# Optimization experiments

Hardware: AMD Instinct MI355X
Metric: run time of the kernel (lower is better)

The kernel has to match this reference:

```python
import jax, jax.numpy as jnp
import numpy as np

KS = 7          # kernel_size (odd)
STRIDE = 2
HALF = KS // 2  # window half-width
B, C, L = 32, 64, 4096


def setup_inputs() -> dict:
    key = jax.random.key(0)
    k1, k2 = jax.random.split(key)
    f = jax.random.normal(k1, (B, C, L), dtype=jnp.float32)
    # learned per-channel scale t ~ U(0, 4) (tiny epsilon to avoid div-by-zero)
    t = jax.random.uniform(k2, (C,), minval=0.0, maxval=4.0, dtype=jnp.float32) + 1e-3
    return {"f": f, "t": t}


def reference(f, t):
    b, c, n = f.shape
    # parabolic structuring function h[c, j] = -z_j^2 / (4 t_c), z = -HALF..HALF
    z = jnp.linspace(-HALF, HALF, KS, dtype=jnp.float32)
    h = -(z ** 2) / (4.0 * t[:, None])  # [C, KS]
    # morphological dilation (max-plus correlation) with -inf padding at borders
    pad = jnp.pad(f, ((0, 0), (0, 0), (HALF, HALF)), constant_values=-jnp.inf)
    out = pad[:, :, 0:n] + h[:, 0][None, :, None]
    for j in range(1, KS):  # small fixed KS-loop; fully vectorized over B,C,L
        out = jnp.maximum(out, pad[:, :, j:j + n] + h[:, j][None, :, None])
    # faithful reproduction of torch.as_strided(out, (B,C,L//stride), (1,1,stride))
    # on the contiguous buffer: element [b,c,i] = out_flat[b + c + i*stride]
    flat = out.reshape(-1)
    idx = (jnp.arange(b)[:, None, None]
           + jnp.arange(c)[None, :, None]
           + jnp.arange(n // STRIDE)[None, None, :] * STRIDE)
    return flat[idx]
```

## Files before the change

### kernel.cpp

```cpp
#include <hip/hip_runtime.h>
#include <math.h>


#define THREADS   256
#define NBLOCKS   512
#define PER_BLOCK 8192
#define NFLAT     4189

__global__ __launch_bounds__(THREADS) void ParabolicPool1DFast_kernel(
    const float* __restrict__ f,
    const float* __restrict__ t,
    float* __restrict__ out)
{
    __shared__ float ev[2096];
    __shared__ float od[2096];

    const int tid = threadIdx.x;
    const float inv4t0 = 0.25f / t[0];
    const float inv4t1 = 0.25f / t[1];

    for (int q = tid; q < NFLAT; q += THREADS) {
        const int c = q >> 12;
        const int l = q & 4095;
        const float* frow = f + (c << 12);
        const float inv4t = c ? inv4t1 : inv4t0;
        float best = -INFINITY;
#pragma unroll
        for (int j = 0; j < 7; ++j) {
            const int z = j - 3;
            const int idx = l + z;
            if (idx >= 0 && idx < 4096) {
                best = fmaxf(best, frow[idx] - (float)(z * z) * inv4t);
            }
        }
        if (q & 1) od[q >> 1] = best;
        else       ev[q >> 1] = best;
    }
    __syncthreads();

    const int base_o = (int)blockIdx.x * PER_BLOCK;
#pragma unroll
    for (int k = 0; k < PER_BLOCK / THREADS; ++k) {
        const int o    = base_o + k * THREADS + tid;
        const int i    = o & 2047;
        const int r    = o >> 11;
        const int base = (r >> 6) + (r & 63);
        const float* tab = (base & 1) ? od : ev;
        out[o] = tab[(base >> 1) + i];
    }
}

extern "C" void kernel_launch(void* const* d_in, const int* in_sizes, int n_in,
                              void* d_out, int out_size, void* d_ws, size_t ws_size,
                              hipStream_t stream) {
    const float* f = (const float*)d_in[0];
    const float* t = (const float*)d_in[1];
    float* out = (float*)d_out;
    ParabolicPool1DFast_kernel<<<NBLOCKS, THREADS, 0, stream>>>(f, t, out);
}
```

Baseline: 89.88 us.

## Vectorize flat-prefix dilation with float4 loads and one output row per block

The first 4096 flat dilation values are now computed with float4 global loads into a 24-element register window per thread. The symmetric parabola taps are folded so each pair shares one max and one subtract. Blocks now number 2048, each writing a single 2048-wide output row with float4 stores, so the per-element row and table selection is hoisted out of the loop. This cuts scalar global and shared traffic and index arithmetic, at the cost of more blocks that each redo the shared-table build.

```diff
diff --git a/kernel.cpp b/kernel.cpp
--- a/kernel.cpp
+++ b/kernel.cpp
@@ -2,51 +2,81 @@
 #include <math.h>
 
 
-#define THREADS   256
-#define NBLOCKS   512
-#define PER_BLOCK 8192
-#define NFLAT     4189
+#define THREADS 256
+#define NBLOCKS 2048
+#define NFLAT   4189
 
 __global__ __launch_bounds__(THREADS) void ParabolicPool1DFast_kernel(
     const float* __restrict__ f,
     const float* __restrict__ t,
     float* __restrict__ out)
 {
-    __shared__ float ev[2096];
-    __shared__ float od[2096];
+    __shared__ __align__(16) float ev[2096];
+    __shared__ __align__(16) float od[2096];
 
     const int tid = threadIdx.x;
-    const float inv4t0 = 0.25f / t[0];
-    const float inv4t1 = 0.25f / t[1];
+    const float a0 = 0.25f / t[0];
+    const float a1 = 0.25f / t[1];
 
-    for (int q = tid; q < NFLAT; q += THREADS) {
-        const int c = q >> 12;
-        const int l = q & 4095;
-        const float* frow = f + (c << 12);
-        const float inv4t = c ? inv4t1 : inv4t0;
+    {
+        const float4* f4 = (const float4*)f;
+        float w[24];
+        const int b0 = 4 * tid - 1;
+#pragma unroll
+        for (int v = 0; v < 6; ++v) {
+            const int fi = b0 + v;
+            const int fic = fi < 0 ? 0 : (fi > 1023 ? 1023 : fi);
+            float4 x = f4[fic];
+            if (fi < 0 || fi > 1023) {
+                x.x = -INFINITY; x.y = -INFINITY; x.z = -INFINITY; x.w = -INFINITY;
+            }
+            w[4*v+0] = x.x; w[4*v+1] = x.y; w[4*v+2] = x.z; w[4*v+3] = x.w;
+        }
+        const float c1 = a0, c2 = 4.0f * a0, c3 = 9.0f * a0;
+        float ve[8], vo[8];
+#pragma unroll
+        for (int p = 0; p < 16; ++p) {
+            const float m1 = fmaxf(w[p+3], w[p+5]);
+            const float m2 = fmaxf(w[p+2], w[p+6]);
+            const float m3 = fmaxf(w[p+1], w[p+7]);
+            const float val = fmaxf(fmaxf(w[p+4], m1 - c1),
+                                    fmaxf(m2 - c2, m3 - c3));
+            if (p & 1) vo[p >> 1] = val;
+            else       ve[p >> 1] = val;
+        }
+        ((float4*)ev)[2*tid]     = make_float4(ve[0], ve[1], ve[2], ve[3]);
+        ((float4*)ev)[2*tid + 1] = make_float4(ve[4], ve[5], ve[6], ve[7]);
+        ((float4*)od)[2*tid]     = make_float4(vo[0], vo[1], vo[2], vo[3]);
+        ((float4*)od)[2*tid + 1] = make_float4(vo[4], vo[5], vo[6], vo[7]);
+    }
+
+    if (tid < NFLAT - 4096) {
+        const float* frow = f + 4096;
         float best = -INFINITY;
 #pragma unroll
         for (int j = 0; j < 7; ++j) {
             const int z = j - 3;
-            const int idx = l + z;
-            if (idx >= 0 && idx < 4096) {
-                best = fmaxf(best, frow[idx] - (float)(z * z) * inv4t);
-            }
+            const int idx = tid + z;
+            if (idx >= 0 && idx < 4096)
+                best = fmaxf(best, frow[idx] - (float)(z * z) * a1);
         }
+        const int q = 4096 + tid;
         if (q & 1) od[q >> 1] = best;
         else       ev[q >> 1] = best;
     }
     __syncthreads();
 
-    const int base_o = (int)blockIdx.x * PER_BLOCK;
+    const int r    = (int)blockIdx.x;
+    const int base = (r >> 6) + (r & 63);
+    const float* tab  = (base & 1) ? od : ev;
+    const int    toff = base >> 1;
+    float* orow = out + (r << 11);
 #pragma unroll
-    for (int k = 0; k < PER_BLOCK / THREADS; ++k) {
-        const int o    = base_o + k * THREADS + tid;
-        const int i    = o & 2047;
-        const int r    = o >> 11;
-        const int base = (r >> 6) + (r & 63);
-        const float* tab = (base & 1) ? od : ev;
-        out[o] = tab[(base >> 1) + i];
+    for (int k = 0; k < 2; ++k) {
+        const int i = (k * THREADS + tid) * 4;
+        const float4 v = make_float4(tab[toff + i],     tab[toff + i + 1],
+                                     tab[toff + i + 2], tab[toff + i + 3]);
+        *(float4*)(orow + i) = v;
     }
 }
 
```

Result: faster. 79.34 us (-11.7%).

## Compute each output row directly with vectorized window loads instead of shared tables

Applied to the files above, without the earlier changes.

Each block now handles one output row (2048 elements). Each thread loads a 24-float window with float4 reads and computes 8 strided outputs in registers using symmetric max pairing. This removes the redundant per-block recomputation of the full 4189-element flat table and the shared-memory staging and sync. The edge case where the window crosses into channel 1 or the array boundary falls back to a scalar path. Output is written with float4 stores.

```diff
diff --git a/kernel.cpp b/kernel.cpp
--- a/kernel.cpp
+++ b/kernel.cpp
@@ -2,52 +2,78 @@
 #include <math.h>
 
 
-#define THREADS   256
-#define NBLOCKS   512
-#define PER_BLOCK 8192
-#define NFLAT     4189
+#define THREADS 256
+#define NBLOCKS 2048
+
+template<int OFF>
+__device__ __forceinline__ void compute8(const float w[24], const float a0,
+                                         float v[8]) {
+#pragma unroll
+    for (int s = 0; s < 8; ++s) {
+        const int c = OFF + 3 + 2 * s;
+        const float m1 = fmaxf(w[c - 1], w[c + 1]);
+        const float m2 = fmaxf(w[c - 2], w[c + 2]);
+        const float m3 = fmaxf(w[c - 3], w[c + 3]);
+        v[s] = fmaxf(fmaxf(w[c], m1 - a0),
+                     fmaxf(m2 - 4.0f * a0, m3 - 9.0f * a0));
+    }
+}
 
 __global__ __launch_bounds__(THREADS) void ParabolicPool1DFast_kernel(
     const float* __restrict__ f,
     const float* __restrict__ t,
     float* __restrict__ out)
 {
-    __shared__ float ev[2096];
-    __shared__ float od[2096];
+    const int tid  = threadIdx.x;
+    const int r    = (int)blockIdx.x;
+    const int base = (r >> 6) + (r & 63);
+    const float a0 = 0.25f / t[0];
 
-    const int tid = threadIdx.x;
-    const float inv4t0 = 0.25f / t[0];
-    const float inv4t1 = 0.25f / t[1];
+    const int Q   = base + 16 * tid;
+    const int off = (base + 1) & 3;
+    const int A   = Q - 3 - off;
 
-    for (int q = tid; q < NFLAT; q += THREADS) {
-        const int c = q >> 12;
-        const int l = q & 4095;
-        const float* frow = f + (c << 12);
-        const float inv4t = c ? inv4t1 : inv4t0;
-        float best = -INFINITY;
+    float v[8];
+    const bool fastp = (A >= 0) && (A + 24 <= 4096) && (Q + 17 <= 4095);
+    if (fastp) {
+        const float4* f4 = (const float4*)f + (A >> 2);
+        float w[24];
 #pragma unroll
-        for (int j = 0; j < 7; ++j) {
-            const int z = j - 3;
-            const int idx = l + z;
-            if (idx >= 0 && idx < 4096) {
-                best = fmaxf(best, frow[idx] - (float)(z * z) * inv4t);
+        for (int k = 0; k < 6; ++k) {
+            const float4 x = f4[k];
+            w[4 * k + 0] = x.x; w[4 * k + 1] = x.y;
+            w[4 * k + 2] = x.z; w[4 * k + 3] = x.w;
+        }
+        switch (off) {
+            case 0:  compute8<0>(w, a0, v); break;
+            case 1:  compute8<1>(w, a0, v); break;
+            case 2:  compute8<2>(w, a0, v); break;
+            default: compute8<3>(w, a0, v); break;
+        }
+    } else {
+        const float a1 = 0.25f / t[1];
+#pragma unroll
+        for (int s = 0; s < 8; ++s) {
+            const int q = Q + 2 * s;
+            const int c = q >> 12;
+            const int l = q & 4095;
+            const float* frow = f + (c << 12);
+            const float aa = c ? a1 : a0;
+            float best = -INFINITY;
+#pragma unroll
+            for (int j = 0; j < 7; ++j) {
+                const int z = j - 3;
+                const int idx = l + z;
+                if (idx >= 0 && idx < 4096)
+                    best = fmaxf(best, frow[idx] - (float)(z * z) * aa);
             }
+            v[s] = best;
         }
-        if (q & 1) od[q >> 1] = best;
-        else       ev[q >> 1] = best;
     }
-    __syncthreads();
 
-    const int base_o = (int)blockIdx.x * PER_BLOCK;
-#pragma unroll
-    for (int k = 0; k < PER_BLOCK / THREADS; ++k) {
-        const int o    = base_o + k * THREADS + tid;
-        const int i    = o & 2047;
-        const int r    = o >> 11;
-        const int base = (r >> 6) + (r & 63);
-        const float* tab = (base & 1) ? od : ev;
-        out[o] = tab[(base >> 1) + i];
-    }
+    float* orow = out + (r << 11) + 8 * tid;
+    *(float4*)(orow)     = make_float4(v[0], v[1], v[2], v[3]);
+    *(float4*)(orow + 4) = make_float4(v[4], v[5], v[6], v[7]);
 }
 
 extern "C" void kernel_launch(void* const* d_in, const int* in_sizes, int n_in,
```

Result: faster. 83.82 us (-6.8%).
